# Performance work log

Hardware: AMD Instinct MI355X
Metric: run time of the kernel (lower is better)

The kernel has to match this reference:

```python
import jax, jax.numpy as jnp
import numpy as np

N_NODES = 32768
N_EDGES = 131072
B = 1024          # number of drug graphs
N_SIDE = 994      # SIDER side effects
SIDE_F = 1050     # glove(300) + label(750)

GAT_DIMS = [(109, 96, 8), (768, 128, 8), (1024, 128, 8), (1024, 128, 1)]  # (in, out_per_head, heads)
LIN_DIMS = [("x5", 128, 64), ("x6", 64, 64), ("w1", 750, 750), ("w2", 750, 64),
            ("z1", 19127, 1600), ("z2", 1600, 64), ("v1", 1024, 256), ("v2", 256, 64),
            ("agg", 192, 64), ("col", 128, 64), ("s1", SIDE_F, 64), ("s2", 64, 64)]


def setup_inputs() -> dict:
    key = jax.random.key(0)
    ks = iter(jax.random.split(key, 64))
    d = {}
    d["x"] = jax.random.normal(next(ks), (N_NODES, 109), jnp.float32)
    d["edge_index"] = jax.random.randint(next(ks), (2, N_EDGES), 0, N_NODES)
    d["batch"] = jnp.arange(N_NODES) // (N_NODES // B)  # 32 atoms per graph
    d["w"] = jax.random.normal(next(ks), (B, 750), jnp.float32)
    d["z"] = jax.random.normal(next(ks), (B, 19127), jnp.float32)
    d["v"] = jax.random.normal(next(ks), (B, 1024), jnp.float32)
    d["side"] = jax.random.normal(next(ks), (N_SIDE, SIDE_F), jnp.float32)
    for i, (fi, fo, h) in enumerate(GAT_DIMS, 1):
        d[f"g{i}_W"] = jax.random.normal(next(ks), (fi, h * fo), jnp.float32) / np.sqrt(fi)
        d[f"g{i}_as"] = jax.random.normal(next(ks), (1, h, fo), jnp.float32) * 0.1
        d[f"g{i}_ad"] = jax.random.normal(next(ks), (1, h, fo), jnp.float32) * 0.1
        d[f"g{i}_b"] = jnp.zeros((h * fo,), jnp.float32)
    for name, fi, fo in LIN_DIMS:
        d[name + "_W"] = jax.random.normal(next(ks), (fi, fo), jnp.float32) / np.sqrt(fi)
        d[name + "_b"] = jnp.zeros((fo,), jnp.float32)
    return d


def _gat(x, src, dst, W, a_s, a_d, b, heads, ch):
    """PyG GATConv (eval mode): linear -> per-edge leaky_relu attention ->
    scatter-softmax over incoming edges (self-loops already in src/dst) -> scatter-sum."""
    N = x.shape[0]
    h = (x @ W).reshape(N, heads, ch)            # [N,H,C]
    al_s = (h * a_s).sum(-1)                     # [N,H]
    al_d = (h * a_d).sum(-1)                     # [N,H]
    e = jax.nn.leaky_relu(al_s[src] + al_d[dst], 0.2)  # [E,H]
    m = jax.ops.segment_max(e, dst, num_segments=N)
    p = jnp.exp(e - m[dst])
    s = jax.ops.segment_sum(p, dst, num_segments=N)
    alpha = p / s[dst]                           # softmax over neighbors of dst
    out = jax.ops.segment_sum(h[src] * alpha[:, :, None], dst, num_segments=N)
    return out.reshape(N, heads * ch) + b


def reference(x, edge_index, batch, w, z, v, side,
              g1_W, g1_as, g1_ad, g1_b, g2_W, g2_as, g2_ad, g2_b,
              g3_W, g3_as, g3_ad, g3_b, g4_W, g4_as, g4_ad, g4_b,
              x5_W, x5_b, x6_W, x6_b, w1_W, w1_b, w2_W, w2_b,
              z1_W, z1_b, z2_W, z2_b, v1_W, v1_b, v2_W, v2_b,
              agg_W, agg_b, col_W, col_b, s1_W, s1_b, s2_W, s2_b):
    relu = jax.nn.relu
    N = x.shape[0]
    nb = w.shape[0]
    loops = jnp.arange(N)
    src = jnp.concatenate([edge_index[0], loops])  # add_self_loops=True (PyG default)
    dst = jnp.concatenate([edge_index[1], loops])
    h = relu(_gat(x, src, dst, g1_W, g1_as, g1_ad, g1_b, 8, 96))
    h = relu(_gat(h, src, dst, g2_W, g2_as, g2_ad, g2_b, 8, 128))
    h = relu(_gat(h, src, dst, g3_W, g3_as, g3_ad, g3_b, 8, 128))
    h = relu(_gat(h, src, dst, g4_W, g4_as, g4_ad, g4_b, 1, 128))
    xg = jax.ops.segment_max(h, batch, num_segments=nb)           # global_max_pool
    xg = relu(relu(xg @ x5_W + x5_b) @ x6_W + x6_b)
    wv = relu(relu(w @ w1_W + w1_b) @ w2_W + w2_b)
    zv = relu(relu(z @ z1_W + z1_b) @ z2_W + z2_b)
    vv = relu(relu(v @ v1_W + v1_b) @ v2_W + v2_b)
    xwz = jnp.concatenate([xg, wv, zv], axis=1) @ agg_W + agg_b   # no activation
    drug = jnp.abs(jnp.tanh(jnp.concatenate([xwz, vv], axis=1) @ col_W + col_b))
    se = jnp.tanh(relu(side @ s1_W + s1_b) @ s2_W + s2_b)
    dn = drug / jnp.maximum(jnp.linalg.norm(drug, axis=1, keepdims=True), 1e-12)
    sn = se / jnp.maximum(jnp.linalg.norm(se, axis=1, keepdims=True), 1e-12)
    freq = 5.0 * (dn @ sn.T)
    return (freq, dn, sn)
```

## Files before the change

### kernel.cpp

```cpp
#include <hip/hip_runtime.h>
#include <math.h>
#include <float.h>

#define E0 131072
#define NN 32768
#define NB 1024
#define NSIDE 994
#define ETOT (E0 + NN)

typedef short bf16x8 __attribute__((ext_vector_type(8)));
typedef unsigned short ushort8 __attribute__((ext_vector_type(8)));
typedef float f32x4 __attribute__((ext_vector_type(4)));

__device__ inline float b2f(unsigned short u) { return __uint_as_float(((unsigned)u) << 16); }
__device__ inline unsigned short f2b(float f) {
  unsigned u = __float_as_uint(f);
  return (unsigned short)((u + 0x7fffu + ((u >> 16) & 1u)) >> 16);
}

__device__ inline void gload_lds16(const void* g, void* l) {
  __builtin_amdgcn_global_load_lds(
      (const __attribute__((address_space(1))) unsigned int*)g,
      (__attribute__((address_space(3))) unsigned int*)l, 16, 0, 0);
}

__global__ void fill_i32(int* p, int v, int n) {
  int i = blockIdx.x * blockDim.x + threadIdx.x;
  if (i < n) p[i] = v;
}

struct CDesc { const float* in; unsigned short* out; int rowsOut, Rreal, C, Cp, wg_end; };
struct CBatch { CDesc d[5]; };
__global__ void conv_batch(CBatch cb) {
  int bid = blockIdx.x;
  int di = 0;
  while (bid >= cb.d[di].wg_end) ++di;
  const CDesc& g = cb.d[di];
  int rel = bid - (di ? cb.d[di - 1].wg_end : 0);
  size_t idx = (size_t)rel * 256 + threadIdx.x;
  size_t tot = (size_t)g.rowsOut * g.Cp;
  if (idx >= tot) return;
  int r = (int)(idx / g.Cp), c = (int)(idx % g.Cp);
  g.out[idx] = (r < g.Rreal && c < g.C) ? f2b(g.in[(size_t)r * g.C + c]) : (unsigned short)0;
}

struct TDesc { const float* W; unsigned short* WT; int K, N, Kp, Npad, gx, wg_end; };
struct TBatch { TDesc d[16]; };
__global__ __launch_bounds__(256) void transpose_batch(TBatch tb) {
  __shared__ float t[32][33];
  int bid = blockIdx.x;
  int di = 0;
  while (bid >= tb.d[di].wg_end) ++di;
  const TDesc& g = tb.d[di];
  int rel = bid - (di ? tb.d[di - 1].wg_end : 0);
  int n0 = (rel % g.gx) * 32, k0 = (rel / g.gx) * 32;
  int tx = threadIdx.x & 31, ty = threadIdx.x >> 5;
  for (int r = ty; r < 32; r += 8) {
    int k = k0 + r, n = n0 + tx;
    t[r][tx] = (k < g.K && n < g.N) ? g.W[(size_t)k * g.N + n] : 0.f;
  }
  __syncthreads();
  for (int r = ty; r < 32; r += 8) {
    int n = n0 + r, k = k0 + tx;
    if (n < g.Npad && k < g.Kp)
      g.WT[(size_t)n * g.Kp + k] = (n < g.N) ? f2b(t[tx][r]) : (unsigned short)0;
  }
}

__global__ void count_deg(const int* __restrict__ ei, int* deg) {
  int e = blockIdx.x * blockDim.x + threadIdx.x;
  if (e >= ETOT) return;
  int dst = (e < E0) ? ei[E0 + e] : (e - E0);
  atomicAdd(&deg[dst], 1);
}

__global__ void scan_deg(const int* __restrict__ deg, int* rowptr, int* cursor) {
  __shared__ int part[1024];
  int tid = threadIdx.x;
  const int chunk = NN / 1024;
  int base = tid * chunk;
  int local[chunk];
  int sum = 0;
#pragma unroll
  for (int i = 0; i < chunk; ++i) { local[i] = sum; sum += deg[base + i]; }
  part[tid] = sum;
  __syncthreads();
  for (int off = 1; off < 1024; off <<= 1) {
    int t = (tid >= off) ? part[tid - off] : 0;
    __syncthreads();
    part[tid] += t;
    __syncthreads();
  }
  int offset = part[tid] - sum;
#pragma unroll
  for (int i = 0; i < chunk; ++i) {
    int v = offset + local[i];
    rowptr[base + i] = v;
    cursor[base + i] = v;
  }
  if (tid == 1023) rowptr[NN] = offset + sum;
}

__global__ void fill_csr(const int* __restrict__ ei, int* cursor,
                         int* __restrict__ srcl, int* __restrict__ pos) {
  int e = blockIdx.x * blockDim.x + threadIdx.x;
  if (e >= ETOT) return;
  int src, dst;
  if (e < E0) { src = ei[e]; dst = ei[E0 + e]; } else { src = dst = e - E0; }
  int p = atomicAdd(&cursor[dst], 1);
  srcl[p] = src;
  pos[e] = p;
}

template <int ACT, int OBF>
__global__ __launch_bounds__(256) void gemm_mfma(
    const unsigned short* __restrict__ A, const unsigned short* __restrict__ BT,
    const float* __restrict__ bias, void* __restrict__ Cp,
    int Nreal, int K, int lda, int ldb, int ldc, int gx, int zpad) {
  __shared__ unsigned short As[2][128 * 32];
  __shared__ unsigned short Bs[2][128 * 32];
  const int nwg = gridDim.x;
  const int chunk = nwg >> 3;
  const int bid = blockIdx.x;
  const int swz = (bid & 7) * chunk + (bid >> 3);
  const int bm = (swz / gx) * 128, bn = (swz % gx) * 128;
  const int tid = threadIdx.x;
  const int wv = tid >> 6, lane = tid & 63;
  const int sr = lane >> 2;
  const int sk = ((lane & 3) ^ ((lane >> 3) & 3)) * 8;
  const int r16 = lane & 15, kq = lane >> 4;
  const int slot8 = (kq ^ ((r16 >> 1) & 3)) * 8;
  const int wr = wv >> 1, wc = wv & 1;
  f32x4 acc[4][4];
#pragma unroll
  for (int i = 0; i < 4; ++i)
#pragma unroll
    for (int j = 0; j < 4; ++j) acc[i][j] = (f32x4){0.f, 0.f, 0.f, 0.f};

  const unsigned short* Abase = A + (size_t)bm * lda;
  const unsigned short* Bbase = BT + (size_t)bn * ldb;
  auto stage = [&](int buf, int k0) {
    gload_lds16(Abase + (size_t)(wv * 16 + sr) * lda + k0 + sk, &As[buf][wv * 512]);
    gload_lds16(Abase + (size_t)(64 + wv * 16 + sr) * lda + k0 + sk, &As[buf][2048 + wv * 512]);
    gload_lds16(Bbase + (size_t)(wv * 16 + sr) * ldb + k0 + sk, &Bs[buf][wv * 512]);
    gload_lds16(Bbase + (size_t)(64 + wv * 16 + sr) * ldb + k0 + sk, &Bs[buf][2048 + wv * 512]);
  };
  stage(0, 0);
  __syncthreads();
  int cur = 0;
  for (int k0 = 0; k0 < K; k0 += 32) {
    if (k0 + 32 < K) stage(cur ^ 1, k0 + 32);
    bf16x8 af[4], bfr[4];
#pragma unroll
    for (int i = 0; i < 4; ++i)
      af[i] = *(const bf16x8*)&As[cur][(wr * 64 + i * 16 + r16) * 32 + slot8];
#pragma unroll
    for (int j = 0; j < 4; ++j)
      bfr[j] = *(const bf16x8*)&Bs[cur][(wc * 64 + j * 16 + r16) * 32 + slot8];
#pragma unroll
    for (int i = 0; i < 4; ++i)
#pragma unroll
      for (int j = 0; j < 4; ++j)
        acc[i][j] = __builtin_amdgcn_mfma_f32_16x16x32_bf16(af[i], bfr[j], acc[i][j], 0, 0, 0);
    __syncthreads();
    cur ^= 1;
  }
#pragma unroll
  for (int i = 0; i < 4; ++i) {
    int row = bm + wr * 64 + i * 16 + kq * 4;
#pragma unroll
    for (int j = 0; j < 4; ++j) {
      int col = bn + wc * 64 + j * 16 + r16;
      bool real = col < Nreal;
      if (!real && !zpad) continue;
      float bv = (bias && real) ? bias[col] : 0.f;
#pragma unroll
      for (int r = 0; r < 4; ++r) {
        float v = acc[i][j][r] + bv;
        if (ACT == 1) v = v > 0.f ? v : 0.f;
        else if (ACT == 2) v = tanhf(v);
        else if (ACT == 3) v = fabsf(tanhf(v));
        if (!real) v = 0.f;
        if (OBF) ((unsigned short*)Cp)[(size_t)(row + r) * ldc + col] = f2b(v);
        else ((float*)Cp)[(size_t)(row + r) * ldc + col] = v;
      }
    }
  }
}

struct GDesc {
  const unsigned short* A; const unsigned short* BT; const float* bias; void* C;
  int Nreal, K, lda, ldb, ldc, gx, zpad, act, obf, wg_end;
};
struct GBatch { GDesc d[5]; };
__global__ __launch_bounds__(256) void gemm_batch(GBatch gb) {
  __shared__ unsigned short As[2][128 * 32];
  __shared__ unsigned short Bs[2][128 * 32];
  int bid = blockIdx.x;
  int di = 0;
  while (bid >= gb.d[di].wg_end) ++di;
  const GDesc& g = gb.d[di];
  int rel = bid - (di ? gb.d[di - 1].wg_end : 0);
  const int bm = (rel / g.gx) * 128, bn = (rel % g.gx) * 128;
  const int tid = threadIdx.x;
  const int wv = tid >> 6, lane = tid & 63;
  const int sr = lane >> 2;
  const int sk = ((lane & 3) ^ ((lane >> 3) & 3)) * 8;
  const int r16 = lane & 15, kq = lane >> 4;
  const int slot8 = (kq ^ ((r16 >> 1) & 3)) * 8;
  const int wr = wv >> 1, wc = wv & 1;
  f32x4 acc[4][4];
#pragma unroll
  for (int i = 0; i < 4; ++i)
#pragma unroll
    for (int j = 0; j < 4; ++j) acc[i][j] = (f32x4){0.f, 0.f, 0.f, 0.f};

  const unsigned short* Abase = g.A + (size_t)bm * g.lda;
  const unsigned short* Bbase = g.BT + (size_t)bn * g.ldb;
  auto stage = [&](int buf, int k0) {
    gload_lds16(Abase + (size_t)(wv * 16 + sr) * g.lda + k0 + sk, &As[buf][wv * 512]);
    gload_lds16(Abase + (size_t)(64 + wv * 16 + sr) * g.lda + k0 + sk, &As[buf][2048 + wv * 512]);
    gload_lds16(Bbase + (size_t)(wv * 16 + sr) * g.ldb + k0 + sk, &Bs[buf][wv * 512]);
    gload_lds16(Bbase + (size_t)(64 + wv * 16 + sr) * g.ldb + k0 + sk, &Bs[buf][2048 + wv * 512]);
  };
  stage(0, 0);
  __syncthreads();
  int cur = 0;
  for (int k0 = 0; k0 < g.K; k0 += 32) {
    if (k0 + 32 < g.K) stage(cur ^ 1, k0 + 32);
    bf16x8 af[4], bfr[4];
#pragma unroll
    for (int i = 0; i < 4; ++i)
      af[i] = *(const bf16x8*)&As[cur][(wr * 64 + i * 16 + r16) * 32 + slot8];
#pragma unroll
    for (int j = 0; j < 4; ++j)
      bfr[j] = *(const bf16x8*)&Bs[cur][(wc * 64 + j * 16 + r16) * 32 + slot8];
#pragma unroll
    for (int i = 0; i < 4; ++i)
#pragma unroll
      for (int j = 0; j < 4; ++j)
        acc[i][j] = __builtin_amdgcn_mfma_f32_16x16x32_bf16(af[i], bfr[j], acc[i][j], 0, 0, 0);
    __syncthreads();
    cur ^= 1;
  }
#pragma unroll
  for (int i = 0; i < 4; ++i) {
    int row = bm + wr * 64 + i * 16 + kq * 4;
#pragma unroll
    for (int j = 0; j < 4; ++j) {
      int col = bn + wc * 64 + j * 16 + r16;
      bool real = col < g.Nreal;
      if (!real && !g.zpad) continue;
      float bv = (g.bias && real) ? g.bias[col] : 0.f;
#pragma unroll
      for (int r = 0; r < 4; ++r) {
        float v = acc[i][j][r] + bv;
        if (g.act == 1) v = v > 0.f ? v : 0.f;
        else if (g.act == 2) v = tanhf(v);
        else if (g.act == 3) v = fabsf(tanhf(v));
        if (!real) v = 0.f;
        if (g.obf) ((unsigned short*)g.C)[(size_t)(row + r) * g.ldc + col] = f2b(v);
        else ((float*)g.C)[(size_t)(row + r) * g.ldc + col] = v;
      }
    }
  }
}

__global__ __launch_bounds__(256) void gemm_mfma_sk(
    const unsigned short* __restrict__ A, const unsigned short* __restrict__ BT,
    float* __restrict__ PART, int lda, int ldb, int ldc) {
  __shared__ unsigned short As[2][128 * 32];
  __shared__ unsigned short Bs[2][128 * 32];
  const int bid = blockIdx.x;
  const int swz = (bid & 7) * 208 + (bid >> 3);
  const int s = swz / 104;
  const int pos = swz - s * 104;
  const int bm = (pos / 13) * 128, bn = (pos % 13) * 128;
  const int base = s * 37 + (s < 6 ? s : 6);
  const int nsteps = 37 + (s < 6 ? 1 : 0);
  const int tid = threadIdx.x;
  const int wv = tid >> 6, lane = tid & 63;
  const int sr = lane >> 2;
  const int sk = ((lane & 3) ^ ((lane >> 3) & 3)) * 8;
  const int r16 = lane & 15, kq = lane >> 4;
  const int slot8 = (kq ^ ((r16 >> 1) & 3)) * 8;
  const int wr = wv >> 1, wc = wv & 1;
  f32x4 acc[4][4];
#pragma unroll
  for (int i = 0; i < 4; ++i)
#pragma unroll
    for (int j = 0; j < 4; ++j) acc[i][j] = (f32x4){0.f, 0.f, 0.f, 0.f};

  const unsigned short* Abase = A + (size_t)bm * lda;
  const unsigned short* Bbase = BT + (size_t)bn * ldb;
  auto stage = [&](int buf, int k0) {
    gload_lds16(Abase + (size_t)(wv * 16 + sr) * lda + k0 + sk, &As[buf][wv * 512]);
    gload_lds16(Abase + (size_t)(64 + wv * 16 + sr) * lda + k0 + sk, &As[buf][2048 + wv * 512]);
    gload_lds16(Bbase + (size_t)(wv * 16 + sr) * ldb + k0 + sk, &Bs[buf][wv * 512]);
    gload_lds16(Bbase + (size_t)(64 + wv * 16 + sr) * ldb + k0 + sk, &Bs[buf][2048 + wv * 512]);
  };
  stage(0, base * 32);
  __syncthreads();
  int cur = 0;
  for (int ks = 0; ks < nsteps; ++ks) {
    if (ks + 1 < nsteps) stage(cur ^ 1, (base + ks + 1) * 32);
    bf16x8 af[4], bfr[4];
#pragma unroll
    for (int i = 0; i < 4; ++i)
      af[i] = *(const bf16x8*)&As[cur][(wr * 64 + i * 16 + r16) * 32 + slot8];
#pragma unroll
    for (int j = 0; j < 4; ++j)
      bfr[j] = *(const bf16x8*)&Bs[cur][(wc * 64 + j * 16 + r16) * 32 + slot8];
#pragma unroll
    for (int i = 0; i < 4; ++i)
#pragma unroll
      for (int j = 0; j < 4; ++j)
        acc[i][j] = __builtin_amdgcn_mfma_f32_16x16x32_bf16(af[i], bfr[j], acc[i][j], 0, 0, 0);
    __syncthreads();
    cur ^= 1;
  }
  float* out = PART + (size_t)s * 1024 * ldc;
#pragma unroll
  for (int i = 0; i < 4; ++i) {
    int row = bm + wr * 64 + i * 16 + kq * 4;
#pragma unroll
    for (int j = 0; j < 4; ++j) {
      int col = bn + wc * 64 + j * 16 + r16;
      if (col >= 1600) continue;
#pragma unroll
      for (int r = 0; r < 4; ++r)
        out[(size_t)(row + r) * ldc + col] = acc[i][j][r];
    }
  }
}

__global__ void zred(const float* __restrict__ PART, const float* __restrict__ bias,
                     unsigned short* __restrict__ ZB) {
  int idx = blockIdx.x * blockDim.x + threadIdx.x;
  if (idx >= 1024 * 1664) return;
  int c = idx % 1664;
  if (c >= 1600) { ZB[idx] = 0; return; }
  float s = 0.f;
#pragma unroll
  for (int k = 0; k < 16; ++k) s += PART[(size_t)k * 1024 * 1664 + idx];
  s += bias[c];
  ZB[idx] = f2b(s > 0.f ? s : 0.f);
}

__global__ void gat_scores_bf(const unsigned short* __restrict__ hlin,
                              const float* __restrict__ a_s, const float* __restrict__ a_d,
                              float* __restrict__ als, float* __restrict__ ald,
                              int H, int C, int tot) {
  int idx = blockIdx.x * blockDim.x + threadIdx.x;
  if (idx >= tot) return;
  int n = idx / H, h = idx - n * H;
  const unsigned short* base = hlin + (size_t)n * H * C + (size_t)h * C;
  const float* as = a_s + h * C;
  const float* ad = a_d + h * C;
  float ss = 0.f, sd = 0.f;
  for (int c = 0; c < C; c += 8) {
    ushort8 v = *(const ushort8*)(base + c);
#pragma unroll
    for (int t = 0; t < 8; ++t) {
      float f = b2f(v[t]);
      ss = fmaf(f, as[c + t], ss);
      sd = fmaf(f, ad[c + t], sd);
    }
  }
  als[idx] = ss;
  ald[idx] = sd;
}

template <int H>
__global__ void edge_attn(const int* __restrict__ ei, const float* __restrict__ als,
                          const float* __restrict__ ald, const int* __restrict__ pos,
                          float* __restrict__ ebs) {
  int e = blockIdx.x * blockDim.x + threadIdx.x;
  if (e >= ETOT) return;
  int src, dst;
  if (e < E0) { src = ei[e]; dst = ei[E0 + e]; } else { src = dst = e - E0; }
  int p = pos[e];
  if (H == 8) {
    float4 s0 = *(const float4*)(als + src * 8);
    float4 s1 = *(const float4*)(als + src * 8 + 4);
    float4 d0 = *(const float4*)(ald + dst * 8);
    float4 d1 = *(const float4*)(ald + dst * 8 + 4);
    float ev[8] = {s0.x + d0.x, s0.y + d0.y, s0.z + d0.z, s0.w + d0.w,
                   s1.x + d1.x, s1.y + d1.y, s1.z + d1.z, s1.w + d1.w};
#pragma unroll
    for (int h = 0; h < 8; ++h) {
      float v = ev[h];
      v = (v >= 0.f) ? v : 0.2f * v;
      ebs[(size_t)p * 8 + h] = __expf(v);
    }
  } else {
    float v = als[src] + ald[dst];
    v = (v >= 0.f) ? v : 0.2f * v;
    ebs[p] = __expf(v);
  }
}

template <int F, int C>
__global__ __launch_bounds__(256) void gat_agg_v3(
    const int* __restrict__ rowptr, const float* __restrict__ ebs,
    const int* __restrict__ srcl, const unsigned short* __restrict__ hlin,
    const float* __restrict__ bias, unsigned short* __restrict__ out) {
  constexpr int H = F / C;
  constexpr int CPN = F / 8;
  int gidx = blockIdx.x * 256 + threadIdx.x;
  if (gidx >= NN * CPN) return;
  int node = gidx / CPN;
  int c0 = (gidx - node * CPN) * 8;
  int h = c0 / C;
  float s = 0.f;
  float acc[8] = {0.f, 0.f, 0.f, 0.f, 0.f, 0.f, 0.f, 0.f};
  int start = rowptr[node], end = rowptr[node + 1];
  for (int k = start; k < end; ++k) {
    int src = srcl[k];
    float p = ebs[(size_t)k * H + h];
    s += p;
    ushort8 hv = *(const ushort8*)(hlin + (size_t)src * F + c0);
#pragma unroll
    for (int t = 0; t < 8; ++t) acc[t] = fmaf(p, b2f(hv[t]), acc[t]);
  }
  float inv_s = 1.f / s;
  ushort8 o;
#pragma unroll
  for (int t = 0; t < 8; ++t) {
    float val = acc[t] * inv_s + bias[c0 + t];
    o[t] = f2b(val > 0.f ? val : 0.f);
  }
  *(ushort8*)(out + (size_t)node * F + c0) = o;
}

__global__ void pool_max(const unsigned short* __restrict__ xb,
                         unsigned short* __restrict__ xgb) {
  int g = blockIdx.x, c = threadIdx.x;
  const unsigned short* base = xb + (size_t)g * 32 * 128 + c;
  float m = -FLT_MAX;
#pragma unroll 8
  for (int n = 0; n < 32; ++n) m = fmaxf(m, b2f(base[n * 128]));
  xgb[g * 128 + c] = f2b(m);
}

__global__ void rownorm2(const float* __restrict__ drug, const float* __restrict__ se,
                         float* __restrict__ dn, float* __restrict__ sn) {
  int b = blockIdx.x, lane = threadIdx.x;
  const float* in; float* outp; int r;
  if (b < NB) { in = drug; outp = dn; r = b; }
  else { in = se; outp = sn; r = b - NB; }
  float v = in[r * 64 + lane];
  float ss = v * v;
#pragma unroll
  for (int off = 1; off < 64; off <<= 1) ss += __shfl_xor(ss, off);
  float nrm = fmaxf(sqrtf(ss), 1e-12f);
  outp[r * 64 + lane] = v / nrm;
}

__global__ __launch_bounds__(256) void freq_k(const float* __restrict__ dn,
                                              const float* __restrict__ sn,
                                              float* __restrict__ C, int M, int N) {
  __shared__ float As[16][64];
  __shared__ float Bs[16][65];
  int tid = threadIdx.x;
  int tx = tid & 15, ty = tid >> 4;
  int bi = blockIdx.y * 16, bj = blockIdx.x * 16;
#pragma unroll
  for (int t = 0; t < 4; ++t) {
    int idx = tid * 4 + t;
    int r = idx >> 6, c = idx & 63;
    As[r][c] = (bi + r < M) ? dn[(bi + r) * 64 + c] : 0.f;
    Bs[r][c] = (bj + r < N) ? sn[(bj + r) * 64 + c] : 0.f;
  }
  __syncthreads();
  float acc = 0.f;
#pragma unroll
  for (int k = 0; k < 64; ++k) acc = fmaf(As[ty][k], Bs[tx][k], acc);
  if (bi + ty < M && bj + tx < N) C[(size_t)(bi + ty) * N + (bj + tx)] = 5.f * acc;
}

extern "C" void kernel_launch(void* const* d_in, const int* in_sizes, int n_in,
                              void* d_out, int out_size, void* d_ws, size_t ws_size,
                              hipStream_t stream) {
  const float* x = (const float*)d_in[0];
  const int* ei = (const int*)d_in[1];
  const float* w = (const float*)d_in[3];
  const float* z = (const float*)d_in[4];
  const float* v = (const float*)d_in[5];
  const float* side = (const float*)d_in[6];
  const float* gW[4] = {(const float*)d_in[7], (const float*)d_in[11],
                        (const float*)d_in[15], (const float*)d_in[19]};
  const float* gas[4] = {(const float*)d_in[8], (const float*)d_in[12],
                         (const float*)d_in[16], (const float*)d_in[20]};
  const float* gad[4] = {(const float*)d_in[9], (const float*)d_in[13],
                         (const float*)d_in[17], (const float*)d_in[21]};
  const float* gb[4] = {(const float*)d_in[10], (const float*)d_in[14],
                        (const float*)d_in[18], (const float*)d_in[22]};
  const float* x5_W = (const float*)d_in[23]; const float* x5_b = (const float*)d_in[24];
  const float* x6_W = (const float*)d_in[25]; const float* x6_b = (const float*)d_in[26];
  const float* w1_W = (const float*)d_in[27]; const float* w1_b = (const float*)d_in[28];
  const float* w2_W = (const float*)d_in[29]; const float* w2_b = (const float*)d_in[30];
  const float* z1_W = (const float*)d_in[31]; const float* z1_b = (const float*)d_in[32];
  const float* z2_W = (const float*)d_in[33]; const float* z2_b = (const float*)d_in[34];
  const float* v1_W = (const float*)d_in[35]; const float* v1_b = (const float*)d_in[36];
  const float* v2_W = (const float*)d_in[37]; const float* v2_b = (const float*)d_in[38];
  const float* agg_W = (const float*)d_in[39]; const float* agg_b = (const float*)d_in[40];
  const float* col_W = (const float*)d_in[41]; const float* col_b = (const float*)d_in[42];
  const float* s1_W = (const float*)d_in[43]; const float* s1_b = (const float*)d_in[44];
  const float* s2_W = (const float*)d_in[45]; const float* s2_b = (const float*)d_in[46];

  char* wsb = (char*)d_ws;
  size_t off = 0;
  auto alloc = [&](size_t bytes) {
    void* p = wsb + off;
    off = (off + bytes + 255) & ~(size_t)255;
    return p;
  };
  unsigned short* HLIN = (unsigned short*)alloc((size_t)NN * 1024 * 2);
  unsigned short* XB = (unsigned short*)alloc((size_t)NN * 1024 * 2);
  unsigned short* WTZ = (unsigned short*)alloc((size_t)1664 * 19136 * 2);
  unsigned short* ZA = (unsigned short*)alloc((size_t)1024 * 19136 * 2);
  unsigned short* WT1 = (unsigned short*)alloc((size_t)768 * 128 * 2);
  unsigned short* WT2 = (unsigned short*)alloc((size_t)1024 * 768 * 2);
  unsigned short* WT3 = (unsigned short*)alloc((size_t)1024 * 1024 * 2);
  unsigned short* WT4 = (unsigned short*)alloc((size_t)128 * 1024 * 2);
  unsigned short* WTW1 = (unsigned short*)alloc((size_t)768 * 768 * 2);
  unsigned short* WTW2 = (unsigned short*)alloc((size_t)128 * 768 * 2);
  unsigned short* WTZ2 = (unsigned short*)alloc((size_t)128 * 1664 * 2);
  unsigned short* WTV1 = (unsigned short*)alloc((size_t)256 * 1024 * 2);
  unsigned short* WTV2 = (unsigned short*)alloc((size_t)128 * 256 * 2);
  unsigned short* WTX5 = (unsigned short*)alloc((size_t)128 * 128 * 2);
  unsigned short* WTX6 = (unsigned short*)alloc((size_t)128 * 64 * 2);
  unsigned short* WTAGG = (unsigned short*)alloc((size_t)128 * 192 * 2);
  unsigned short* WTCOL = (unsigned short*)alloc((size_t)128 * 128 * 2);
  unsigned short* WTS1 = (unsigned short*)alloc((size_t)128 * 1056 * 2);
  unsigned short* WTS2 = (unsigned short*)alloc((size_t)128 * 64 * 2);
  unsigned short* WB = (unsigned short*)alloc((size_t)1024 * 768 * 2);
  unsigned short* VB = (unsigned short*)alloc((size_t)1024 * 1024 * 2);
  unsigned short* SIDEB = (unsigned short*)alloc((size_t)1024 * 1056 * 2);
  unsigned short* XGB = (unsigned short*)alloc((size_t)1024 * 128 * 2);
  unsigned short* ZB = (unsigned short*)alloc((size_t)1024 * 1664 * 2);
  unsigned short* X5O = (unsigned short*)alloc((size_t)1024 * 128 * 2);
  unsigned short* WMID = (unsigned short*)alloc((size_t)1024 * 768 * 2);
  unsigned short* VMID = (unsigned short*)alloc((size_t)1024 * 256 * 2);
  unsigned short* SEMID = (unsigned short*)alloc((size_t)1024 * 128 * 2);
  unsigned short* CAT192 = (unsigned short*)alloc((size_t)1024 * 192 * 2);
  unsigned short* CAT128 = (unsigned short*)alloc((size_t)1024 * 128 * 2);
  float* EBS = (float*)alloc((size_t)ETOT * 8 * 4);
  float* ALS = (float*)alloc((size_t)NN * 8 * 4);
  float* ALD = (float*)alloc((size_t)NN * 8 * 4);
  float* DRUG = (float*)alloc((size_t)NB * 64 * 4);
  float* SE = (float*)alloc((size_t)1024 * 64 * 4);
  int* DEG = (int*)alloc((size_t)NN * 4);
  int* ROWPTR = (int*)alloc((size_t)(NN + 1) * 4);
  int* CURSOR = (int*)alloc((size_t)NN * 4);
  int* SRCL = (int*)alloc((size_t)ETOT * 4);
  int* POS = (int*)alloc((size_t)ETOT * 4);
  float* PART = (float*)HLIN;

  hipLaunchKernelGGL(fill_i32, dim3((NN + 255) / 256), dim3(256), 0, stream, DEG, 0, NN);
  hipLaunchKernelGGL(count_deg, dim3((ETOT + 255) / 256), dim3(256), 0, stream, ei, DEG);
  hipLaunchKernelGGL(scan_deg, dim3(1), dim3(1024), 0, stream, DEG, ROWPTR, CURSOR);
  hipLaunchKernelGGL(fill_csr, dim3((ETOT + 255) / 256), dim3(256), 0, stream, ei, CURSOR, SRCL, POS);

  {
    TBatch tb;
    int acc_wg = 0, i = 0;
    auto add = [&](const float* W, unsigned short* WT, int K, int N, int Kp, int Npad) {
      int gx = Npad / 32, gy = Kp / 32;
      acc_wg += gx * gy;
      tb.d[i++] = {W, WT, K, N, Kp, Npad, gx, acc_wg};
    };
    add(z1_W, WTZ, 19127, 1600, 19136, 1664);
    add(gW[0], WT1, 109, 768, 128, 768);
    add(gW[1], WT2, 768, 1024, 768, 1024);
    add(gW[2], WT3, 1024, 1024, 1024, 1024);
    add(gW[3], WT4, 1024, 128, 1024, 128);
    add(w1_W, WTW1, 750, 750, 768, 768);
    add(w2_W, WTW2, 750, 64, 768, 128);
    add(z2_W, WTZ2, 1600, 64, 1664, 128);
    add(v1_W, WTV1, 1024, 256, 1024, 256);
    add(v2_W, WTV2, 256, 64, 256, 128);
    add(x5_W, WTX5, 128, 64, 128, 128);
    add(x6_W, WTX6, 64, 64, 64, 128);
    add(agg_W, WTAGG, 192, 64, 192, 128);
    add(col_W, WTCOL, 128, 64, 128, 128);
    add(s1_W, WTS1, 1050, 64, 1056, 128);
    add(s2_W, WTS2, 64, 64, 64, 128);
    hipLaunchKernelGGL(transpose_batch, dim3(acc_wg), dim3(256), 0, stream, tb);
  }

  {
    CBatch cb;
    int acc_wg = 0, i = 0;
    auto add = [&](const float* in, unsigned short* out, int rowsOut, int Rreal, int C, int Cp) {
      acc_wg += (int)(((size_t)rowsOut * Cp + 255) / 256);
      cb.d[i++] = {in, out, rowsOut, Rreal, C, Cp, acc_wg};
    };
    add(z, ZA, NB, NB, 19127, 19136);
    add(x, XB, NN, NN, 109, 128);
    add(w, WB, 1024, 1024, 750, 768);
    add(v, VB, 1024, 1024, 1024, 1024);
    add(side, SIDEB, 1024, 994, 1050, 1056);
    hipLaunchKernelGGL(conv_batch, dim3(acc_wg), dim3(256), 0, stream, cb);
  }

  auto mm = [&](const unsigned short* A, const unsigned short* BT,
                const float* bias, void* C, int M, int Npad, int Nreal, int K,
                int lda, int ldb, int ldc, int zpad) {
    int gx = Npad / 128;
    int nwg = gx * (M / 128);
    hipLaunchKernelGGL((gemm_mfma<0, 1>), dim3(nwg), dim3(256), 0, stream,
                       A, BT, bias, C, Nreal, K, lda, ldb, ldc, gx, zpad);
  };

  const int Hs[4] = {8, 8, 8, 1};
  const int Kp[4] = {128, 768, 1024, 1024};
  const unsigned short* WTs[4] = {WT1, WT2, WT3, WT4};
  const int Fs[4] = {768, 1024, 1024, 128};
  for (int l = 0; l < 4; ++l) {
    int H = Hs[l], F = Fs[l], C = F / H;
    mm(XB, WTs[l], nullptr, HLIN, NN, F, F, Kp[l], Kp[l], Kp[l], F, 0);
    int totNH = NN * H;
    hipLaunchKernelGGL(gat_scores_bf, dim3((totNH + 255) / 256), dim3(256), 0, stream,
                       HLIN, gas[l], gad[l], ALS, ALD, H, C, totNH);
    if (H == 8)
      hipLaunchKernelGGL((edge_attn<8>), dim3((ETOT + 255) / 256), dim3(256), 0, stream, ei, ALS, ALD, POS, EBS);
    else
      hipLaunchKernelGGL((edge_attn<1>), dim3((ETOT + 255) / 256), dim3(256), 0, stream, ei, ALS, ALD, POS, EBS);
    if (l == 0)
      hipLaunchKernelGGL((gat_agg_v3<768, 96>), dim3(NN * 96 / 256), dim3(256), 0, stream,
                         ROWPTR, EBS, SRCL, HLIN, gb[l], XB);
    else if (l == 3)
      hipLaunchKernelGGL((gat_agg_v3<128, 128>), dim3(NN * 16 / 256), dim3(256), 0, stream,
                         ROWPTR, EBS, SRCL, HLIN, gb[l], XB);
    else
      hipLaunchKernelGGL((gat_agg_v3<1024, 128>), dim3(NN * 128 / 256), dim3(256), 0, stream,
                         ROWPTR, EBS, SRCL, HLIN, gb[l], XB);
  }

  hipLaunchKernelGGL(pool_max, dim3(NB), dim3(128), 0, stream, XB, XGB);

  {
    GBatch b;
    int acc_wg = 0, i = 0;
    auto add = [&](const unsigned short* A, const unsigned short* BT, const float* bias,
                   void* C, int Npad, int Nreal, int K, int lda, int ldb, int ldc,
                   int zpad, int act, int obf) {
      int gx = Npad / 128;
      acc_wg += gx * 8;
      b.d[i++] = {A, BT, bias, C, Nreal, K, lda, ldb, ldc, gx, zpad, act, obf, acc_wg};
    };
    add(WB, WTW1, w1_b, WMID, 768, 750, 768, 768, 768, 768, 1, 1, 1);
    add(VB, WTV1, v1_b, VMID, 256, 256, 1024, 1024, 1024, 256, 0, 1, 1);
    add(SIDEB, WTS1, s1_b, SEMID, 128, 64, 1056, 1056, 1056, 128, 1, 1, 1);
    add(XGB, WTX5, x5_b, X5O, 128, 64, 128, 128, 128, 128, 1, 1, 1);
    while (i < 5) { b.d[i] = b.d[i - 1]; b.d[i].wg_end = acc_wg; ++i; }
    hipLaunchKernelGGL(gemm_batch, dim3(acc_wg), dim3(256), 0, stream, b);
  }

  hipLaunchKernelGGL(gemm_mfma_sk, dim3(1664), dim3(256), 0, stream, ZA, WTZ, PART, 19136, 19136, 1664);
  hipLaunchKernelGGL(zred, dim3((1024 * 1664 + 255) / 256), dim3(256), 0, stream, PART, z1_b, ZB);

  {
    GBatch b;
    int acc_wg = 0, i = 0;
    auto add = [&](const unsigned short* A, const unsigned short* BT, const float* bias,
                   void* C, int Npad, int Nreal, int K, int lda, int ldb, int ldc,
                   int zpad, int act, int obf) {
      int gx = Npad / 128;
      acc_wg += gx * 8;
      b.d[i++] = {A, BT, bias, C, Nreal, K, lda, ldb, ldc, gx, zpad, act, obf, acc_wg};
    };
    add(X5O, WTX6, x6_b, CAT192 + 0, 128, 64, 64, 128, 64, 192, 0, 1, 1);
    add(WMID, WTW2, w2_b, CAT192 + 64, 128, 64, 768, 768, 768, 192, 0, 1, 1);
    add(ZB, WTZ2, z2_b, CAT192 + 128, 128, 64, 1664, 1664, 1664, 192, 0, 1, 1);
    add(VMID, WTV2, v2_b, CAT128 + 64, 128, 64, 256, 256, 256, 128, 0, 1, 1);
    add(SEMID, WTS2, s2_b, SE, 128, 64, 64, 128, 64, 64, 0, 2, 0);
    hipLaunchKernelGGL(gemm_batch, dim3(acc_wg), dim3(256), 0, stream, b);
  }

  {
    GBatch b;
    b.d[0] = {CAT192, WTAGG, agg_b, CAT128 + 0, 64, 192, 192, 192, 128, 1, 0, 0, 1, 8};
    for (int i = 1; i < 5; ++i) { b.d[i] = b.d[0]; }
    hipLaunchKernelGGL(gemm_batch, dim3(8), dim3(256), 0, stream, b);
  }
  {
    GBatch b;
    b.d[0] = {CAT128, WTCOL, col_b, DRUG, 64, 128, 128, 128, 64, 1, 0, 3, 0, 8};
    for (int i = 1; i < 5; ++i) { b.d[i] = b.d[0]; }
    hipLaunchKernelGGL(gemm_batch, dim3(8), dim3(256), 0, stream, b);
  }

  float* outp = (float*)d_out;
  float* DN = outp + (size_t)NB * NSIDE;
  float* SN = DN + (size_t)NB * 64;
  hipLaunchKernelGGL(rownorm2, dim3(NB + NSIDE), dim3(64), 0, stream, DRUG, SE, DN, SN);
  hipLaunchKernelGGL(freq_k, dim3((NSIDE + 15) / 16, (NB + 15) / 16), dim3(256), 0, stream,
                     DN, SN, outp, NB, NSIDE);
}
```

Measured before the change: 1.035 ms.

## Fuse tail GEMMs with row-normalization, store split-K partials in bf16

Merges the agg and col GEMMs plus the drug row-norm into a single kernel that keeps the intermediate in LDS. It also folds the side-effect tanh and L2-normalization into the batched GEMM epilogue through a new act mode. The z1 split-K partials are now stored in bf16 rather than fp32, and the reduction reads them as 8-wide vectors, which halves partial-sum traffic at some cost in accuracy. The split-K kernel drops LDS double buffering, which cuts LDS use but gives up overlap of loads with compute.

```diff
diff --git a/kernel.cpp b/kernel.cpp
--- a/kernel.cpp
+++ b/kernel.cpp
@@ -190,7 +190,7 @@
 
 struct GDesc {
   const unsigned short* A; const unsigned short* BT; const float* bias; void* C;
-  int Nreal, K, lda, ldb, ldc, gx, zpad, act, obf, wg_end;
+  int Nreal, K, lda, ldb, ldc, gx, zpad, act, obf, Mreal, wg_end;
 };
 struct GBatch { GDesc d[5]; };
 __global__ __launch_bounds__(256) void gemm_batch(GBatch gb) {
@@ -243,6 +243,30 @@
     __syncthreads();
     cur ^= 1;
   }
+  if (g.act == 4) {
+    if (wc == 0) {
+#pragma unroll
+      for (int i = 0; i < 4; ++i)
+#pragma unroll
+        for (int r = 0; r < 4; ++r) {
+          int row = bm + wr * 64 + i * 16 + kq * 4 + r;
+          float vv[4];
+#pragma unroll
+          for (int j = 0; j < 4; ++j) vv[j] = tanhf(acc[i][j][r] + g.bias[j * 16 + r16]);
+          float ss = vv[0] * vv[0] + vv[1] * vv[1] + vv[2] * vv[2] + vv[3] * vv[3];
+          ss += __shfl_xor(ss, 1);
+          ss += __shfl_xor(ss, 2);
+          ss += __shfl_xor(ss, 4);
+          ss += __shfl_xor(ss, 8);
+          float inv = 1.f / fmaxf(sqrtf(ss), 1e-12f);
+          if (row < g.Mreal)
+#pragma unroll
+            for (int j = 0; j < 4; ++j)
+              ((float*)g.C)[(size_t)row * g.ldc + j * 16 + r16] = vv[j] * inv;
+        }
+    }
+    return;
+  }
 #pragma unroll
   for (int i = 0; i < 4; ++i) {
     int row = bm + wr * 64 + i * 16 + kq * 4;
@@ -268,9 +292,9 @@
 
 __global__ __launch_bounds__(256) void gemm_mfma_sk(
     const unsigned short* __restrict__ A, const unsigned short* __restrict__ BT,
-    float* __restrict__ PART, int lda, int ldb, int ldc) {
-  __shared__ unsigned short As[2][128 * 32];
-  __shared__ unsigned short Bs[2][128 * 32];
+    unsigned short* __restrict__ PART, int lda, int ldb, int ldc) {
+  __shared__ unsigned short As[128 * 32];
+  __shared__ unsigned short Bs[128 * 32];
   const int bid = blockIdx.x;
   const int swz = (bid & 7) * 208 + (bid >> 3);
   const int s = swz / 104;
@@ -293,33 +317,28 @@
 
   const unsigned short* Abase = A + (size_t)bm * lda;
   const unsigned short* Bbase = BT + (size_t)bn * ldb;
-  auto stage = [&](int buf, int k0) {
-    gload_lds16(Abase + (size_t)(wv * 16 + sr) * lda + k0 + sk, &As[buf][wv * 512]);
-    gload_lds16(Abase + (size_t)(64 + wv * 16 + sr) * lda + k0 + sk, &As[buf][2048 + wv * 512]);
-    gload_lds16(Bbase + (size_t)(wv * 16 + sr) * ldb + k0 + sk, &Bs[buf][wv * 512]);
-    gload_lds16(Bbase + (size_t)(64 + wv * 16 + sr) * ldb + k0 + sk, &Bs[buf][2048 + wv * 512]);
-  };
-  stage(0, base * 32);
-  __syncthreads();
-  int cur = 0;
   for (int ks = 0; ks < nsteps; ++ks) {
-    if (ks + 1 < nsteps) stage(cur ^ 1, (base + ks + 1) * 32);
+    int k0 = (base + ks) * 32;
+    gload_lds16(Abase + (size_t)(wv * 16 + sr) * lda + k0 + sk, &As[wv * 512]);
+    gload_lds16(Abase + (size_t)(64 + wv * 16 + sr) * lda + k0 + sk, &As[2048 + wv * 512]);
+    gload_lds16(Bbase + (size_t)(wv * 16 + sr) * ldb + k0 + sk, &Bs[wv * 512]);
+    gload_lds16(Bbase + (size_t)(64 + wv * 16 + sr) * ldb + k0 + sk, &Bs[2048 + wv * 512]);
+    __syncthreads();
     bf16x8 af[4], bfr[4];
 #pragma unroll
     for (int i = 0; i < 4; ++i)
-      af[i] = *(const bf16x8*)&As[cur][(wr * 64 + i * 16 + r16) * 32 + slot8];
+      af[i] = *(const bf16x8*)&As[(wr * 64 + i * 16 + r16) * 32 + slot8];
 #pragma unroll
     for (int j = 0; j < 4; ++j)
-      bfr[j] = *(const bf16x8*)&Bs[cur][(wc * 64 + j * 16 + r16) * 32 + slot8];
+      bfr[j] = *(const bf16x8*)&Bs[(wc * 64 + j * 16 + r16) * 32 + slot8];
 #pragma unroll
     for (int i = 0; i < 4; ++i)
 #pragma unroll
       for (int j = 0; j < 4; ++j)
         acc[i][j] = __builtin_amdgcn_mfma_f32_16x16x32_bf16(af[i], bfr[j], acc[i][j], 0, 0, 0);
     __syncthreads();
-    cur ^= 1;
-  }
-  float* out = PART + (size_t)s * 1024 * ldc;
+  }
+  unsigned short* out = PART + (size_t)s * 1024 * ldc;
 #pragma unroll
   for (int i = 0; i < 4; ++i) {
     int row = bm + wr * 64 + i * 16 + kq * 4;
@@ -329,22 +348,143 @@
       if (col >= 1600) continue;
 #pragma unroll
       for (int r = 0; r < 4; ++r)
-        out[(size_t)(row + r) * ldc + col] = acc[i][j][r];
+        out[(size_t)(row + r) * ldc + col] = f2b(acc[i][j][r]);
     }
   }
 }
 
-__global__ void zred(const float* __restrict__ PART, const float* __restrict__ bias,
+__global__ void zred(const unsigned short* __restrict__ PART, const float* __restrict__ bias,
                      unsigned short* __restrict__ ZB) {
-  int idx = blockIdx.x * blockDim.x + threadIdx.x;
-  if (idx >= 1024 * 1664) return;
-  int c = idx % 1664;
-  if (c >= 1600) { ZB[idx] = 0; return; }
-  float s = 0.f;
-#pragma unroll
-  for (int k = 0; k < 16; ++k) s += PART[(size_t)k * 1024 * 1664 + idx];
-  s += bias[c];
-  ZB[idx] = f2b(s > 0.f ? s : 0.f);
+  int g = blockIdx.x * blockDim.x + threadIdx.x;
+  if (g >= 1024 * 1664 / 8) return;
+  size_t base = (size_t)g * 8;
+  int c0 = (int)(base % 1664);
+  ushort8 o;
+  if (c0 >= 1600) {
+#pragma unroll
+    for (int t = 0; t < 8; ++t) o[t] = 0;
+  } else {
+    float s[8] = {0.f, 0.f, 0.f, 0.f, 0.f, 0.f, 0.f, 0.f};
+#pragma unroll
+    for (int k = 0; k < 16; ++k) {
+      ushort8 p = *(const ushort8*)&PART[(size_t)k * 1024 * 1664 + base];
+#pragma unroll
+      for (int t = 0; t < 8; ++t) s[t] += b2f(p[t]);
+    }
+#pragma unroll
+    for (int t = 0; t < 8; ++t) {
+      float v = s[t] + bias[c0 + t];
+      o[t] = f2b(v > 0.f ? v : 0.f);
+    }
+  }
+  *(ushort8*)&ZB[base] = o;
+}
+
+__global__ __launch_bounds__(256) void tail_fused(
+    const unsigned short* __restrict__ CAT192, const unsigned short* __restrict__ WTAGG,
+    const float* __restrict__ agg_b, const unsigned short* __restrict__ CAT128,
+    const unsigned short* __restrict__ WTCOL, const float* __restrict__ col_b,
+    float* __restrict__ DN) {
+  __shared__ unsigned short S1[128 * 32];
+  __shared__ unsigned short S2[128 * 32];
+  __shared__ unsigned short ACAT[128 * 128];
+  const int bm = blockIdx.x * 128;
+  const int tid = threadIdx.x;
+  const int wv = tid >> 6, lane = tid & 63;
+  const int sr = lane >> 2;
+  const int sk = ((lane & 3) ^ ((lane >> 3) & 3)) * 8;
+  const int r16 = lane & 15, kq = lane >> 4;
+  const int slot8 = (kq ^ ((r16 >> 1) & 3)) * 8;
+  const int wr = wv >> 1, wc = wv & 1;
+  f32x4 acc[4][4];
+#pragma unroll
+  for (int i = 0; i < 4; ++i)
+#pragma unroll
+    for (int j = 0; j < 4; ++j) acc[i][j] = (f32x4){0.f, 0.f, 0.f, 0.f};
+
+  const unsigned short* Abase = CAT192 + (size_t)bm * 192;
+  for (int k0 = 0; k0 < 192; k0 += 32) {
+    gload_lds16(Abase + (size_t)(wv * 16 + sr) * 192 + k0 + sk, &S1[wv * 512]);
+    gload_lds16(Abase + (size_t)(64 + wv * 16 + sr) * 192 + k0 + sk, &S1[2048 + wv * 512]);
+    gload_lds16(WTAGG + (size_t)(wv * 16 + sr) * 192 + k0 + sk, &S2[wv * 512]);
+    gload_lds16(WTAGG + (size_t)(64 + wv * 16 + sr) * 192 + k0 + sk, &S2[2048 + wv * 512]);
+    __syncthreads();
+    bf16x8 af[4], bfr[4];
+#pragma unroll
+    for (int i = 0; i < 4; ++i)
+      af[i] = *(const bf16x8*)&S1[(wr * 64 + i * 16 + r16) * 32 + slot8];
+#pragma unroll
+    for (int j = 0; j < 4; ++j)
+      bfr[j] = *(const bf16x8*)&S2[(wc * 64 + j * 16 + r16) * 32 + slot8];
+#pragma unroll
+    for (int i = 0; i < 4; ++i)
+#pragma unroll
+      for (int j = 0; j < 4; ++j)
+        acc[i][j] = __builtin_amdgcn_mfma_f32_16x16x32_bf16(af[i], bfr[j], acc[i][j], 0, 0, 0);
+    __syncthreads();
+  }
+  if (wc == 0) {
+#pragma unroll
+    for (int i = 0; i < 4; ++i)
+#pragma unroll
+      for (int j = 0; j < 4; ++j) {
+        int col = j * 16 + r16;
+#pragma unroll
+        for (int r = 0; r < 4; ++r) {
+          int rl = wr * 64 + i * 16 + kq * 4 + r;
+          ACAT[rl * 128 + col] = f2b(acc[i][j][r] + agg_b[col]);
+        }
+      }
+  }
+  for (int idx = tid; idx < 128 * 8; idx += 256) {
+    int row = idx >> 3, c8 = (idx & 7) * 8;
+    *(ushort8*)&ACAT[row * 128 + 64 + c8] =
+        *(const ushort8*)&CAT128[(size_t)(bm + row) * 128 + 64 + c8];
+  }
+#pragma unroll
+  for (int i = 0; i < 4; ++i)
+#pragma unroll
+    for (int j = 0; j < 4; ++j) acc[i][j] = (f32x4){0.f, 0.f, 0.f, 0.f};
+  __syncthreads();
+
+  for (int k0 = 0; k0 < 128; k0 += 32) {
+    gload_lds16(WTCOL + (size_t)(wv * 16 + sr) * 128 + k0 + sk, &S1[wv * 512]);
+    gload_lds16(WTCOL + (size_t)(64 + wv * 16 + sr) * 128 + k0 + sk, &S1[2048 + wv * 512]);
+    __syncthreads();
+    bf16x8 af[4], bfr[4];
+#pragma unroll
+    for (int i = 0; i < 4; ++i)
+      af[i] = *(const bf16x8*)&ACAT[(wr * 64 + i * 16 + r16) * 128 + k0 + kq * 8];
+#pragma unroll
+    for (int j = 0; j < 4; ++j)
+      bfr[j] = *(const bf16x8*)&S1[(wc * 64 + j * 16 + r16) * 32 + slot8];
+#pragma unroll
+    for (int i = 0; i < 4; ++i)
+#pragma unroll
+      for (int j = 0; j < 4; ++j)
+        acc[i][j] = __builtin_amdgcn_mfma_f32_16x16x32_bf16(af[i], bfr[j], acc[i][j], 0, 0, 0);
+    __syncthreads();
+  }
+  if (wc == 0) {
+#pragma unroll
+    for (int i = 0; i < 4; ++i)
+#pragma unroll
+      for (int r = 0; r < 4; ++r) {
+        int row = bm + wr * 64 + i * 16 + kq * 4 + r;
+        float vv[4];
+#pragma unroll
+        for (int j = 0; j < 4; ++j) vv[j] = fabsf(tanhf(acc[i][j][r] + col_b[j * 16 + r16]));
+        float ss = vv[0] * vv[0] + vv[1] * vv[1] + vv[2] * vv[2] + vv[3] * vv[3];
+        ss += __shfl_xor(ss, 1);
+        ss += __shfl_xor(ss, 2);
+        ss += __shfl_xor(ss, 4);
+        ss += __shfl_xor(ss, 8);
+        float inv = 1.f / fmaxf(sqrtf(ss), 1e-12f);
+#pragma unroll
+        for (int j = 0; j < 4; ++j)
+          DN[(size_t)row * 64 + j * 16 + r16] = vv[j] * inv;
+      }
+  }
 }
 
 __global__ void gat_scores_bf(const unsigned short* __restrict__ hlin,
@@ -441,20 +581,6 @@
 #pragma unroll 8
   for (int n = 0; n < 32; ++n) m = fmaxf(m, b2f(base[n * 128]));
   xgb[g * 128 + c] = f2b(m);
-}
-
-__global__ void rownorm2(const float* __restrict__ drug, const float* __restrict__ se,
-                         float* __restrict__ dn, float* __restrict__ sn) {
-  int b = blockIdx.x, lane = threadIdx.x;
-  const float* in; float* outp; int r;
-  if (b < NB) { in = drug; outp = dn; r = b; }
-  else { in = se; outp = sn; r = b - NB; }
-  float v = in[r * 64 + lane];
-  float ss = v * v;
-#pragma unroll
-  for (int off = 1; off < 64; off <<= 1) ss += __shfl_xor(ss, off);
-  float nrm = fmaxf(sqrtf(ss), 1e-12f);
-  outp[r * 64 + lane] = v / nrm;
 }
 
 __global__ __launch_bounds__(256) void freq_k(const float* __restrict__ dn,
@@ -549,14 +675,12 @@
   float* EBS = (float*)alloc((size_t)ETOT * 8 * 4);
   float* ALS = (float*)alloc((size_t)NN * 8 * 4);
   float* ALD = (float*)alloc((size_t)NN * 8 * 4);
-  float* DRUG = (float*)alloc((size_t)NB * 64 * 4);
-  float* SE = (float*)alloc((size_t)1024 * 64 * 4);
   int* DEG = (int*)alloc((size_t)NN * 4);
   int* ROWPTR = (int*)alloc((size_t)(NN + 1) * 4);
   int* CURSOR = (int*)alloc((size_t)NN * 4);
   int* SRCL = (int*)alloc((size_t)ETOT * 4);
   int* POS = (int*)alloc((size_t)ETOT * 4);
-  float* PART = (float*)HLIN;
+  unsigned short* PART = (unsigned short*)HLIN;
 
   hipLaunchKernelGGL(fill_i32, dim3((NN + 255) / 256), dim3(256), 0, stream, DEG, 0, NN);
   hipLaunchKernelGGL(count_deg, dim3((ETOT + 255) / 256), dim3(256), 0, stream, ei, DEG);
@@ -646,57 +770,47 @@
     int acc_wg = 0, i = 0;
     auto add = [&](const unsigned short* A, const unsigned short* BT, const float* bias,
                    void* C, int Npad, int Nreal, int K, int lda, int ldb, int ldc,
-                   int zpad, int act, int obf) {
+                   int zpad, int act, int obf, int Mreal) {
       int gx = Npad / 128;
       acc_wg += gx * 8;
-      b.d[i++] = {A, BT, bias, C, Nreal, K, lda, ldb, ldc, gx, zpad, act, obf, acc_wg};
+      b.d[i++] = {A, BT, bias, C, Nreal, K, lda, ldb, ldc, gx, zpad, act, obf, Mreal, acc_wg};
     };
-    add(WB, WTW1, w1_b, WMID, 768, 750, 768, 768, 768, 768, 1, 1, 1);
-    add(VB, WTV1, v1_b, VMID, 256, 256, 1024, 1024, 1024, 256, 0, 1, 1);
-    add(SIDEB, WTS1, s1_b, SEMID, 128, 64, 1056, 1056, 1056, 128, 1, 1, 1);
-    add(XGB, WTX5, x5_b, X5O, 128, 64, 128, 128, 128, 128, 1, 1, 1);
+    add(WB, WTW1, w1_b, WMID, 768, 750, 768, 768, 768, 768, 1, 1, 1, 1024);
+    add(VB, WTV1, v1_b, VMID, 256, 256, 1024, 1024, 1024, 256, 0, 1, 1, 1024);
+    add(SIDEB, WTS1, s1_b, SEMID, 128, 64, 1056, 1056, 1056, 128, 1, 1, 1, 1024);
+    add(XGB, WTX5, x5_b, X5O, 128, 64, 128, 128, 128, 128, 1, 1, 1, 1024);
     while (i < 5) { b.d[i] = b.d[i - 1]; b.d[i].wg_end = acc_wg; ++i; }
     hipLaunchKernelGGL(gemm_batch, dim3(acc_wg), dim3(256), 0, stream, b);
   }
 
   hipLaunchKernelGGL(gemm_mfma_sk, dim3(1664), dim3(256), 0, stream, ZA, WTZ, PART, 19136, 19136, 1664);
-  hipLaunchKernelGGL(zred, dim3((1024 * 1664 + 255) / 256), dim3(256), 0, stream, PART, z1_b, ZB);
+  hipLaunchKernelGGL(zred, dim3((1024 * 1664 / 8 + 255) / 256), dim3(256), 0, stream, PART, z1_b, ZB);
+
+  float* outp = (float*)d_out;
+  float* DN = outp + (size_t)NB * NSIDE;
+  float* SN = DN + (size_t)NB * 64;
 
   {
     GBatch b;
     int acc_wg = 0, i = 0;
     auto add = [&](const unsigned short* A, const unsigned short* BT, const float* bias,
                    void* C, int Npad, int Nreal, int K, int lda, int ldb, int ldc,
-                   int zpad, int act, int obf) {
+                   int zpad, int act, int obf, int Mreal) {
       int gx = Npad / 128;
       acc_wg += gx * 8;
-      b.d[i++] = {A, BT, bias, C, Nreal, K, lda, ldb, ldc, gx, zpad, act, obf, acc_wg};
+      b.d[i++] = {A, BT, bias, C, Nreal, K, lda, ldb, ldc, gx, zpad, act, obf, Mreal, acc_wg};
     };
-    add(X5O, WTX6, x6_b, CAT192 + 0, 128, 64, 64, 128, 64, 192, 0, 1, 1);
-    add(WMID, WTW2, w2_b, CAT192 + 64, 128, 64, 768, 768, 768, 192, 0, 1, 1);
-    add(ZB, WTZ2, z2_b, CAT192 + 128, 128, 64, 1664, 1664, 1664, 192, 0, 1, 1);
-    add(VMID, WTV2, v2_b, CAT128 + 64, 128, 64, 256, 256, 256, 128, 0, 1, 1);
-    add(SEMID, WTS2, s2_b, SE, 128, 64, 64, 128, 64, 64, 0, 2, 0);
+    add(X5O, WTX6, x6_b, CAT192 + 0, 128, 64, 64, 128, 64, 192, 0, 1, 1, 1024);
+    add(WMID, WTW2, w2_b, CAT192 + 64, 128, 64, 768, 768, 768, 192, 0, 1, 1, 1024);
+    add(ZB, WTZ2, z2_b, CAT192 + 128, 128, 64, 1664, 1664, 1664, 192, 0, 1, 1, 1024);
+    add(VMID, WTV2, v2_b, CAT128 + 64, 128, 64, 256, 256, 256, 128, 0, 1, 1, 1024);
+    add(SEMID, WTS2, s2_b, SN, 128, 64, 64, 128, 64, 64, 0, 4, 0, 994);
     hipLaunchKernelGGL(gemm_batch, dim3(acc_wg), dim3(256), 0, stream, b);
   }
 
-  {
-    GBatch b;
-    b.d[0] = {CAT192, WTAGG, agg_b, CAT128 + 0, 64, 192, 192, 192, 128, 1, 0, 0, 1, 8};
-    for (int i = 1; i < 5; ++i) { b.d[i] = b.d[0]; }
-    hipLaunchKernelGGL(gemm_batch, dim3(8), dim3(256), 0, stream, b);
-  }
-  {
-    GBatch b;
-    b.d[0] = {CAT128, WTCOL, col_b, DRUG, 64, 128, 128, 128, 64, 1, 0, 3, 0, 8};
-    for (int i = 1; i < 5; ++i) { b.d[i] = b.d[0]; }
-    hipLaunchKernelGGL(gemm_batch, dim3(8), dim3(256), 0, stream, b);
-  }
-
-  float* outp = (float*)d_out;
-  float* DN = outp + (size_t)NB * NSIDE;
-  float* SN = DN + (size_t)NB * 64;
-  hipLaunchKernelGGL(rownorm2, dim3(NB + NSIDE), dim3(64), 0, stream, DRUG, SE, DN, SN);
+  hipLaunchKernelGGL(tail_fused, dim3(8), dim3(256), 0, stream,
+                     CAT192, WTAGG, agg_b, CAT128, WTCOL, col_b, DN);
+
   hipLaunchKernelGGL(freq_k, dim3((NSIDE + 15) / 16, (NB + 15) / 16), dim3(256), 0, stream,
                      DN, SN, outp, NB, NSIDE);
 }
```

Result: faster. 1.010 ms (-2.4%).
